# Kernel optimization log

Hardware: AMD Instinct MI355X
Metric: run time of the kernel (lower is better)

The kernel has to match this reference:

```python
import jax, jax.numpy as jnp
import numpy as np

NUM_ANCHORS_LIST = [6400, 1600, 400]  # 640x640 input, strides 8/16/32
STRIDES = [8, 16, 32]
GRID_SIZES = [80, 40, 20]
TOPK = 9
EPS = 1e-9


def _make_anchor_bboxes():
    boxes = []
    for stride, size in zip(STRIDES, GRID_SIZES):
        c = (np.arange(size, dtype=np.float32) + 0.5) * stride
        cx, cy = np.meshgrid(c, c)
        half = stride / 2.0
        b = np.stack([cx - half, cy - half, cx + half, cy + half], axis=-1)
        boxes.append(b.reshape(-1, 4))
    return jnp.asarray(np.concatenate(boxes, axis=0))  # [8400,4]


def _random_boxes(key, shape_prefix, img=640.0):
    k1, k2 = jax.random.split(key)
    cxy = jax.random.uniform(k1, shape_prefix + (2,), minval=0.0, maxval=img)
    wh = jax.random.uniform(k2, shape_prefix + (2,), minval=8.0, maxval=160.0)
    x1y1 = jnp.clip(cxy - wh / 2, 0.0, img)
    x2y2 = jnp.clip(cxy + wh / 2, 0.0, img)
    return jnp.concatenate([x1y1, x2y2], axis=-1).astype(jnp.float32)


def setup_inputs() -> dict:
    key = jax.random.key(0)
    kg, kp, kl, km = jax.random.split(key, 4)
    B, N, M, C = 16, 8400, 128, 80
    return {
        "anchor_bboxes": _make_anchor_bboxes(),               # [N,4]
        "gt_labels": jax.random.randint(kl, (B, M, 1), 0, C).astype(jnp.int64),
        "gt_bboxes": _random_boxes(kg, (B, M)),               # [B,M,4]
        "mask_gt": jax.random.randint(km, (B, M, 1), 0, 2).astype(jnp.int32),
        "pred_bboxes": _random_boxes(kp, (B, N)),             # [B,N,4]
        "num_classes": C,
    }


def _batch_bbox_iou(box1, box2):
    # box1 [B,N,4], box2 [B,M,4] -> [B,N,M]
    area1 = (box1[..., 2] - box1[..., 0]) * (box1[..., 3] - box1[..., 1])
    area2 = (box2[..., 2] - box2[..., 0]) * (box2[..., 3] - box2[..., 1])
    ix1 = jnp.maximum(box1[:, :, None, 0], box2[:, None, :, 0])
    iy1 = jnp.maximum(box1[:, :, None, 1], box2[:, None, :, 1])
    ix2 = jnp.minimum(box1[:, :, None, 2], box2[:, None, :, 2])
    iy2 = jnp.minimum(box1[:, :, None, 3], box2[:, None, :, 3])
    inter = jnp.maximum(ix2 - ix1, 0.0) * jnp.maximum(iy2 - iy1, 0.0)
    union = area1[:, :, None] + area2[:, None, :] - inter
    return inter / (union + EPS)


def reference(anchor_bboxes, gt_labels, gt_bboxes, mask_gt, pred_bboxes, num_classes):
    B, M = gt_bboxes.shape[0], gt_bboxes.shape[1]
    N = anchor_bboxes.shape[0]
    labels = gt_labels[..., 0].astype(jnp.int32)           # [B,M]

    ac = (anchor_bboxes[:, :2] + anchor_bboxes[:, 2:]) / 2  # [N,2]
    gc = (gt_bboxes[..., :2] + gt_bboxes[..., 2:]) / 2      # [B,M,2]
    # cdist via expanded quadratic form (avoids [B,N,M,2] intermediate)
    a2 = jnp.sum(ac * ac, axis=-1)                          # [N]
    g2 = jnp.sum(gc * gc, axis=-1)                          # [B,M]
    d2 = a2[None, :, None] + g2[:, None, :] - 2.0 * jnp.einsum('nc,bmc->bnm', ac, gc)
    distances = jnp.sqrt(jnp.maximum(d2, 0.0))              # [B,N,M]

    # per-level topk closest anchors per GT -> candidate mask [B,N,M]
    bidx = jnp.arange(B)[:, None, None]
    midx = jnp.arange(M)[None, :, None]
    level_masks = []
    start = 0
    for ln in NUM_ANCHORS_LIST:
        ld = distances[:, start:start + ln, :]               # [B,ln,M]
        k = min(TOPK, ln)
        _, idx = jax.lax.top_k(-jnp.swapaxes(ld, 1, 2), k)   # [B,M,k] anchor idx
        lm = jnp.zeros((B, ln, M), dtype=bool).at[bidx, idx, midx].set(True)
        level_masks.append(lm)
        start += ln
    candidate_mask = jnp.concatenate(level_masks, axis=1)    # [B,N,M]

    ious = _batch_bbox_iou(jnp.broadcast_to(anchor_bboxes[None], (B, N, 4)), gt_bboxes)
    cm_f = candidate_mask.astype(ious.dtype)
    cand_ious = ious * cm_f
    count = jnp.maximum(cm_f.sum(axis=1), 1.0)               # [B,M]
    mean = cand_ious.sum(axis=1) / count
    sq_mean = jnp.sum(cand_ious * cand_ious, axis=1) / count # mask is 0/1
    std = jnp.sqrt(jnp.maximum(sq_mean - mean * mean, 0.0))
    thr = mean + std                                         # [B,M]

    is_pos = candidate_mask & (ious >= thr[:, None, :])
    center_in_gt = ((ac[None, :, None, 0] >= gt_bboxes[:, None, :, 0])
                    & (ac[None, :, None, 0] <= gt_bboxes[:, None, :, 2])
                    & (ac[None, :, None, 1] >= gt_bboxes[:, None, :, 1])
                    & (ac[None, :, None, 1] <= gt_bboxes[:, None, :, 3]))
    is_pos = is_pos & center_in_gt & (mask_gt[..., 0] > 0)[:, None, :]

    fg_mask = jnp.any(is_pos, axis=-1)                       # [B,N]
    pos_ious = jnp.where(is_pos, ious, 0.0)
    max_gt_idx = jnp.argmax(pos_ious, axis=-1)               # [B,N]

    fg_f = fg_mask.astype(ious.dtype)
    assigned_labels = jnp.take_along_axis(labels, max_gt_idx, axis=1) * fg_mask.astype(jnp.int32)
    assigned_bboxes = jnp.take_along_axis(gt_bboxes, max_gt_idx[..., None], axis=1) * fg_f[..., None]
    assigned_ious = jnp.take_along_axis(ious, max_gt_idx[..., None], axis=2)[..., 0] * fg_f

    pred_ious = _batch_bbox_iou(pred_bboxes, gt_bboxes)
    pred_assigned = jnp.take_along_axis(pred_ious, max_gt_idx[..., None], axis=2)[..., 0] * fg_f
    assigned_ious = assigned_ious * pred_assigned

    assigned_scores = jax.nn.one_hot(assigned_labels, num_classes, dtype=ious.dtype) \
        * (assigned_ious * fg_f)[..., None]                  # [B,N,C]
    return assigned_labels, assigned_bboxes, assigned_scores, fg_mask
```

## Files before the change

kernel.cpp:

```cpp
#include <hip/hip_runtime.h>
#include <stdint.h>

#define B_ 16
#define N_ 8400
#define M_ 128
#define SC4_  2688000
#define ZB_   512
#define ZPER_ 5250

__device__ __forceinline__ float iou_box(float ax1, float ay1, float ax2, float ay2,
                                         float bx1, float by1, float bx2, float by2) {
    float area1 = __fmul_rn(__fsub_rn(ax2, ax1), __fsub_rn(ay2, ay1));
    float area2 = __fmul_rn(__fsub_rn(bx2, bx1), __fsub_rn(by2, by1));
    float ix1 = fmaxf(ax1, bx1), iy1 = fmaxf(ay1, by1);
    float ix2 = fminf(ax2, bx2), iy2 = fminf(ay2, by2);
    float iw = fmaxf(__fsub_rn(ix2, ix1), 0.0f);
    float ih = fmaxf(__fsub_rn(iy2, iy1), 0.0f);
    float inter = __fmul_rn(iw, ih);
    float uni = __fsub_rn(__fadd_rn(area1, area2), inter);
    return __fdiv_rn(inter, __fadd_rn(uni, 1e-9f));
}

__global__ __launch_bounds__(256) void assign_zero_kernel(
    const float* __restrict__ gt_bboxes,
    const int* __restrict__ mask_gt,
    unsigned long long* __restrict__ ws,
    float* __restrict__ out) {
    if (blockIdx.x >= 2048) {
        float4* sp = (float4*)(out + (size_t)B_ * N_ * 5) +
                     (size_t)(blockIdx.x - 2048) * ZPER_;
        const float4 z4 = make_float4(0.f, 0.f, 0.f, 0.f);
        for (int k = threadIdx.x; k < ZPER_; k += 256) sp[k] = z4;
        return;
    }

    const int g = blockIdx.x;
    if (mask_gt[g] == 0) return;
    const int t = threadIdx.x;
    if (t >= 192) return;
    const int b = g >> 7;
    const int m = g & (M_ - 1);
    const int w = t >> 6;
    const int lane = t & 63;

    __shared__ int   s_idx[27];
    __shared__ float s_iou[27];
    __shared__ int   s_cin[27];
    __shared__ float s_thr;

    const float4 gb = ((const float4*)gt_bboxes)[g];
    const float gx1 = gb.x, gy1 = gb.y, gx2 = gb.z, gy2 = gb.w;
    const float gcx = __fmul_rn(__fadd_rn(gx1, gx2), 0.5f);
    const float gcy = __fmul_rn(__fadd_rn(gy1, gy2), 0.5f);
    const float g2 = __fadd_rn(__fmul_rn(gcx, gcx), __fmul_rn(gcy, gcy));

    const int   size  = (w == 0) ? 80 : ((w == 1) ? 40 : 20);
    const int   start = (w == 0) ? 0 : ((w == 1) ? 6400 : 8000);
    const float st    = (w == 0) ? 8.0f : ((w == 1) ? 16.0f : 32.0f);
    const float inv   = (w == 0) ? 0.125f : ((w == 1) ? 0.0625f : 0.03125f);

    int jl = (int)floorf(gcx * inv - 0.5f) - 2;
    int il = (int)floorf(gcy * inv - 0.5f) - 2;
    jl = min(max(jl, 0), size - 6);
    il = min(max(il, 0), size - 6);

    unsigned long long key = ~0ULL;
    if (lane < 36) {
        const int wy = lane / 6;
        const int wx = lane - wy * 6;
        const int   i   = il + wy;
        const int   j   = jl + wx;
        const float acy = __fmul_rn(__fadd_rn((float)i, 0.5f), st);
        const float acx = __fmul_rn(__fadd_rn((float)j, 0.5f), st);
        const int   n   = start + i * size + j;
        float a2  = __fadd_rn(__fmul_rn(acx, acx), __fmul_rn(acy, acy));
        float dot = __fadd_rn(__fmul_rn(acx, gcx), __fmul_rn(acy, gcy));
        float d2  = __fsub_rn(__fadd_rn(a2, g2), __fmul_rn(2.0f, dot));
        float dist = __fsqrt_rn(fmaxf(d2, 0.0f));
        key = ((unsigned long long)__float_as_uint(dist) << 32) | (unsigned)n;
    }

#pragma unroll
    for (int k = 2; k <= 64; k <<= 1) {
#pragma unroll
        for (int j = k >> 1; j > 0; j >>= 1) {
            unsigned long long other = __shfl_xor(key, j, 64);
            const bool up = ((lane & k) == 0);
            const bool keepMin = (((lane & j) == 0) == up);
            const unsigned long long mn = key < other ? key : other;
            const unsigned long long mx = key < other ? other : key;
            key = keepMin ? mn : mx;
        }
    }
    if (lane < 9) s_idx[w * 9 + lane] = (int)(key & 0xFFFFFFFFu);
    __syncthreads();

    if (t < 3) {
        int v[9];
#pragma unroll
        for (int k = 0; k < 9; ++k) v[k] = s_idx[t * 9 + k];
#pragma unroll
        for (int rr = 0; rr < 9; ++rr) {
#pragma unroll
            for (int p = (rr & 1); p + 1 < 9; p += 2) {
                int lo = min(v[p], v[p + 1]);
                int hi = max(v[p], v[p + 1]);
                v[p] = lo; v[p + 1] = hi;
            }
        }
#pragma unroll
        for (int k = 0; k < 9; ++k) s_idx[t * 9 + k] = v[k];
    }
    __syncthreads();

    if (t < 27) {
        const int   l      = t / 9;
        const int   size2  = (l == 0) ? 80 : ((l == 1) ? 40 : 20);
        const int   start2 = (l == 0) ? 0 : ((l == 1) ? 6400 : 8000);
        const float st2    = (l == 0) ? 8.0f : ((l == 1) ? 16.0f : 32.0f);
        const float half   = __fmul_rn(st2, 0.5f);
        const int n = s_idx[t];
        const int loc = n - start2;
        const int i = loc / size2;
        const int j = loc - i * size2;
        float acx = __fmul_rn(__fadd_rn((float)j, 0.5f), st2);
        float acy = __fmul_rn(__fadd_rn((float)i, 0.5f), st2);
        float ax1 = __fsub_rn(acx, half), ay1 = __fsub_rn(acy, half);
        float ax2 = __fadd_rn(acx, half), ay2 = __fadd_rn(acy, half);
        float iou = iou_box(ax1, ay1, ax2, ay2, gx1, gy1, gx2, gy2);
        s_iou[t] = iou;
        s_cin[t] = (acx >= gx1 && acx <= gx2 && acy >= gy1 && acy <= gy2) ? 1 : 0;
    }
    __syncthreads();

    if (t == 0) {
        float tot = 0.0f, tot2 = 0.0f;
#pragma unroll
        for (int kk = 0; kk < 27; ++kk) {
            const float iou = s_iou[kk];
            tot  = __fadd_rn(tot, iou);
            tot2 = __fadd_rn(tot2, __fmul_rn(iou, iou));
        }
        float mean = __fdiv_rn(tot, 27.0f);
        float sqm  = __fdiv_rn(tot2, 27.0f);
        float var  = __fsub_rn(sqm, __fmul_rn(mean, mean));
        float stdv = __fsqrt_rn(fmaxf(var, 0.0f));
        s_thr = __fadd_rn(mean, stdv);
    }
    __syncthreads();

    if (t < 27) {
        const float iou = s_iou[t];
        if (s_cin[t] && iou >= s_thr) {
            unsigned long long packed =
                ((unsigned long long)(0xC0000000u | __float_as_uint(iou)) << 32) |
                (unsigned long long)(0xFFFFFFFFu - (unsigned)m);
            atomicMax(&ws[(size_t)b * N_ + s_idx[t]], packed);
        }
    }
}

__global__ __launch_bounds__(256) void finalize_kernel(
    const int* __restrict__ gt_labels,
    const float* __restrict__ gt_bboxes,
    const float* __restrict__ pred_bboxes,
    const int* __restrict__ num_classes_p,
    const unsigned long long* __restrict__ ws,
    float* __restrict__ out) {
    const int idx = blockIdx.x * 256 + threadIdx.x;
    const int b = idx / N_;
    const int C = num_classes_p[0];

    const unsigned long long w = ws[idx];
    const bool fg = (w >> 62) == 3ULL;
    float labelf = 0.0f;
    float4 bb = make_float4(0.f, 0.f, 0.f, 0.f);
    float v = 0.0f, fgf = 0.0f;
    int label = 0;
    if (fg) {
        fgf = 1.0f;
        const unsigned mm = 0xFFFFFFFFu - (unsigned)(w & 0xFFFFFFFFu);
        const float a_iou = __uint_as_float((unsigned)((w >> 32) & 0x3FFFFFFFu));
        label = gt_labels[b * M_ + (int)mm];
        labelf = (float)label;
        const float* gg = gt_bboxes + ((size_t)b * M_ + mm) * 4;
        bb.x = gg[0]; bb.y = gg[1]; bb.z = gg[2]; bb.w = gg[3];
        const float* p = pred_bboxes + (size_t)idx * 4;
        float piou = iou_box(p[0], p[1], p[2], p[3], bb.x, bb.y, bb.z, bb.w);
        v = __fmul_rn(a_iou, piou);
    }

    out[idx] = labelf;
    ((float4*)(out + (size_t)B_ * N_))[idx] = bb;
    if (fg) out[(size_t)B_ * N_ * 5 + (size_t)idx * C + label] = v;
    out[(size_t)B_ * N_ * (5 + C) + idx] = fgf;
}

extern "C" void kernel_launch(void* const* d_in, const int* in_sizes, int n_in,
                              void* d_out, int out_size, void* d_ws, size_t ws_size,
                              hipStream_t stream) {
    const int*   gt_labels  = (const int*)d_in[1];
    const float* gt_bboxes  = (const float*)d_in[2];
    const int*   mask_gt    = (const int*)d_in[3];
    const float* pred       = (const float*)d_in[4];
    const int*   ncls       = (const int*)d_in[5];
    unsigned long long* ws  = (unsigned long long*)d_ws;
    float* out              = (float*)d_out;

    assign_zero_kernel<<<2048 + ZB_, 256, 0, stream>>>(gt_bboxes, mask_gt, ws, out);
    finalize_kernel<<<(B_ * N_) / 256, 256, 0, stream>>>(
        gt_labels, gt_bboxes, pred, ncls, ws, out);
}
```

Baseline: 82.91 us.

## Fuse assignment, output zeroing, and finalize into one cooperative kernel

Merges the per-GT assignment kernel and the per-anchor finalize kernel into a single cooperative launch of 2048 blocks. A grid-wide sync separates the two phases. Zeroing of the whole output now happens in each block's fourth wave, alongside the assignment work. The finalize phase now writes only foreground anchors because everything was pre-zeroed. This removes one kernel launch and the dense writes of background entries, at the cost of a grid barrier and a requirement that all 2048 blocks be co-resident.

```diff
diff --git a/kernel.cpp b/kernel.cpp
--- a/kernel.cpp
+++ b/kernel.cpp
@@ -1,12 +1,14 @@
 #include <hip/hip_runtime.h>
+#include <hip/hip_cooperative_groups.h>
 #include <stdint.h>
+
+namespace cg = cooperative_groups;
 
 #define B_ 16
 #define N_ 8400
 #define M_ 128
-#define SC4_  2688000
-#define ZB_   512
-#define ZPER_ 5250
+#define OUT4_ 2889600
+#define ZPER_ 1411
 
 __device__ __forceinline__ float iou_box(float ax1, float ay1, float ax2, float ay2,
                                          float bx1, float by1, float bx2, float by2) {
@@ -21,81 +23,90 @@
     return __fdiv_rn(inter, __fadd_rn(uni, 1e-9f));
 }
 
-__global__ __launch_bounds__(256) void assign_zero_kernel(
+__global__ __launch_bounds__(256, 8) void fused_coop_kernel(
+    const int* __restrict__ gt_labels,
     const float* __restrict__ gt_bboxes,
     const int* __restrict__ mask_gt,
+    const float* __restrict__ pred_bboxes,
+    const int* __restrict__ num_classes_p,
     unsigned long long* __restrict__ ws,
     float* __restrict__ out) {
-    if (blockIdx.x >= 2048) {
-        float4* sp = (float4*)(out + (size_t)B_ * N_ * 5) +
-                     (size_t)(blockIdx.x - 2048) * ZPER_;
-        const float4 z4 = make_float4(0.f, 0.f, 0.f, 0.f);
-        for (int k = threadIdx.x; k < ZPER_; k += 256) sp[k] = z4;
-        return;
-    }
-
+    cg::grid_group grid = cg::this_grid();
     const int g = blockIdx.x;
-    if (mask_gt[g] == 0) return;
     const int t = threadIdx.x;
-    if (t >= 192) return;
+    const bool activeGT = (mask_gt[g] != 0);
     const int b = g >> 7;
     const int m = g & (M_ - 1);
-    const int w = t >> 6;
-    const int lane = t & 63;
 
     __shared__ int   s_idx[27];
     __shared__ float s_iou[27];
     __shared__ int   s_cin[27];
     __shared__ float s_thr;
 
-    const float4 gb = ((const float4*)gt_bboxes)[g];
-    const float gx1 = gb.x, gy1 = gb.y, gx2 = gb.z, gy2 = gb.w;
-    const float gcx = __fmul_rn(__fadd_rn(gx1, gx2), 0.5f);
-    const float gcy = __fmul_rn(__fadd_rn(gy1, gy2), 0.5f);
-    const float g2 = __fadd_rn(__fmul_rn(gcx, gcx), __fmul_rn(gcy, gcy));
-
-    const int   size  = (w == 0) ? 80 : ((w == 1) ? 40 : 20);
-    const int   start = (w == 0) ? 0 : ((w == 1) ? 6400 : 8000);
-    const float st    = (w == 0) ? 8.0f : ((w == 1) ? 16.0f : 32.0f);
-    const float inv   = (w == 0) ? 0.125f : ((w == 1) ? 0.0625f : 0.03125f);
-
-    int jl = (int)floorf(gcx * inv - 0.5f) - 2;
-    int il = (int)floorf(gcy * inv - 0.5f) - 2;
-    jl = min(max(jl, 0), size - 6);
-    il = min(max(il, 0), size - 6);
-
-    unsigned long long key = ~0ULL;
-    if (lane < 36) {
-        const int wy = lane / 6;
-        const int wx = lane - wy * 6;
-        const int   i   = il + wy;
-        const int   j   = jl + wx;
-        const float acy = __fmul_rn(__fadd_rn((float)i, 0.5f), st);
-        const float acx = __fmul_rn(__fadd_rn((float)j, 0.5f), st);
-        const int   n   = start + i * size + j;
-        float a2  = __fadd_rn(__fmul_rn(acx, acx), __fmul_rn(acy, acy));
-        float dot = __fadd_rn(__fmul_rn(acx, gcx), __fmul_rn(acy, gcy));
-        float d2  = __fsub_rn(__fadd_rn(a2, g2), __fmul_rn(2.0f, dot));
-        float dist = __fsqrt_rn(fmaxf(d2, 0.0f));
-        key = ((unsigned long long)__float_as_uint(dist) << 32) | (unsigned)n;
-    }
-
-#pragma unroll
-    for (int k = 2; k <= 64; k <<= 1) {
-#pragma unroll
-        for (int j = k >> 1; j > 0; j >>= 1) {
-            unsigned long long other = __shfl_xor(key, j, 64);
-            const bool up = ((lane & k) == 0);
-            const bool keepMin = (((lane & j) == 0) == up);
-            const unsigned long long mn = key < other ? key : other;
-            const unsigned long long mx = key < other ? other : key;
-            key = keepMin ? mn : mx;
-        }
-    }
-    if (lane < 9) s_idx[w * 9 + lane] = (int)(key & 0xFFFFFFFFu);
-    __syncthreads();
-
-    if (t < 3) {
+    float gx1 = 0.f, gy1 = 0.f, gx2 = 0.f, gy2 = 0.f;
+    if (activeGT) {
+        const float4 gb = ((const float4*)gt_bboxes)[g];
+        gx1 = gb.x; gy1 = gb.y; gx2 = gb.z; gy2 = gb.w;
+    }
+
+    if (t >= 192) {
+        float4* o4 = (float4*)out;
+        const float4 z4 = make_float4(0.f, 0.f, 0.f, 0.f);
+        const int base = g * ZPER_;
+        for (int k = t - 192; k < ZPER_; k += 64) {
+            const int i = base + k;
+            if (i < OUT4_) o4[i] = z4;
+        }
+    } else if (activeGT) {
+        const int w = t >> 6;
+        const int lane = t & 63;
+        const float gcx = __fmul_rn(__fadd_rn(gx1, gx2), 0.5f);
+        const float gcy = __fmul_rn(__fadd_rn(gy1, gy2), 0.5f);
+        const float g2 = __fadd_rn(__fmul_rn(gcx, gcx), __fmul_rn(gcy, gcy));
+
+        const int   size  = (w == 0) ? 80 : ((w == 1) ? 40 : 20);
+        const int   start = (w == 0) ? 0 : ((w == 1) ? 6400 : 8000);
+        const float st    = (w == 0) ? 8.0f : ((w == 1) ? 16.0f : 32.0f);
+        const float inv   = (w == 0) ? 0.125f : ((w == 1) ? 0.0625f : 0.03125f);
+
+        int jl = (int)floorf(gcx * inv - 0.5f) - 2;
+        int il = (int)floorf(gcy * inv - 0.5f) - 2;
+        jl = min(max(jl, 0), size - 6);
+        il = min(max(il, 0), size - 6);
+
+        unsigned long long key = ~0ULL;
+        if (lane < 36) {
+            const int wy = lane / 6;
+            const int wx = lane - wy * 6;
+            const int   i   = il + wy;
+            const int   j   = jl + wx;
+            const float acy = __fmul_rn(__fadd_rn((float)i, 0.5f), st);
+            const float acx = __fmul_rn(__fadd_rn((float)j, 0.5f), st);
+            const int   n   = start + i * size + j;
+            float a2  = __fadd_rn(__fmul_rn(acx, acx), __fmul_rn(acy, acy));
+            float dot = __fadd_rn(__fmul_rn(acx, gcx), __fmul_rn(acy, gcy));
+            float d2  = __fsub_rn(__fadd_rn(a2, g2), __fmul_rn(2.0f, dot));
+            float dist = __fsqrt_rn(fmaxf(d2, 0.0f));
+            key = ((unsigned long long)__float_as_uint(dist) << 32) | (unsigned)n;
+        }
+
+#pragma unroll
+        for (int k = 2; k <= 64; k <<= 1) {
+#pragma unroll
+            for (int j = k >> 1; j > 0; j >>= 1) {
+                unsigned long long other = __shfl_xor(key, j, 64);
+                const bool up = ((lane & k) == 0);
+                const bool keepMin = (((lane & j) == 0) == up);
+                const unsigned long long mn = key < other ? key : other;
+                const unsigned long long mx = key < other ? other : key;
+                key = keepMin ? mn : mx;
+            }
+        }
+        if (lane < 9) s_idx[w * 9 + lane] = (int)(key & 0xFFFFFFFFu);
+    }
+    __syncthreads();
+
+    if (activeGT && t < 3) {
         int v[9];
 #pragma unroll
         for (int k = 0; k < 9; ++k) v[k] = s_idx[t * 9 + k];
@@ -113,7 +124,7 @@
     }
     __syncthreads();
 
-    if (t < 27) {
+    if (activeGT && t < 27) {
         const int   l      = t / 9;
         const int   size2  = (l == 0) ? 80 : ((l == 1) ? 40 : 20);
         const int   start2 = (l == 0) ? 0 : ((l == 1) ? 6400 : 8000);
@@ -133,7 +144,7 @@
     }
     __syncthreads();
 
-    if (t == 0) {
+    if (activeGT && t == 0) {
         float tot = 0.0f, tot2 = 0.0f;
 #pragma unroll
         for (int kk = 0; kk < 27; ++kk) {
@@ -149,7 +160,7 @@
     }
     __syncthreads();
 
-    if (t < 27) {
+    if (activeGT && t < 27) {
         const float iou = s_iou[t];
         if (s_cin[t] && iou >= s_thr) {
             unsigned long long packed =
@@ -158,42 +169,32 @@
             atomicMax(&ws[(size_t)b * N_ + s_idx[t]], packed);
         }
     }
-}
-
-__global__ __launch_bounds__(256) void finalize_kernel(
-    const int* __restrict__ gt_labels,
-    const float* __restrict__ gt_bboxes,
-    const float* __restrict__ pred_bboxes,
-    const int* __restrict__ num_classes_p,
-    const unsigned long long* __restrict__ ws,
-    float* __restrict__ out) {
-    const int idx = blockIdx.x * 256 + threadIdx.x;
-    const int b = idx / N_;
+
+    grid.sync();
+
     const int C = num_classes_p[0];
-
-    const unsigned long long w = ws[idx];
-    const bool fg = (w >> 62) == 3ULL;
-    float labelf = 0.0f;
-    float4 bb = make_float4(0.f, 0.f, 0.f, 0.f);
-    float v = 0.0f, fgf = 0.0f;
-    int label = 0;
-    if (fg) {
-        fgf = 1.0f;
-        const unsigned mm = 0xFFFFFFFFu - (unsigned)(w & 0xFFFFFFFFu);
-        const float a_iou = __uint_as_float((unsigned)((w >> 32) & 0x3FFFFFFFu));
-        label = gt_labels[b * M_ + (int)mm];
-        labelf = (float)label;
-        const float* gg = gt_bboxes + ((size_t)b * M_ + mm) * 4;
-        bb.x = gg[0]; bb.y = gg[1]; bb.z = gg[2]; bb.w = gg[3];
-        const float* p = pred_bboxes + (size_t)idx * 4;
-        float piou = iou_box(p[0], p[1], p[2], p[3], bb.x, bb.y, bb.z, bb.w);
-        v = __fmul_rn(a_iou, piou);
-    }
-
-    out[idx] = labelf;
-    ((float4*)(out + (size_t)B_ * N_))[idx] = bb;
-    if (fg) out[(size_t)B_ * N_ * 5 + (size_t)idx * C + label] = v;
-    out[(size_t)B_ * N_ * (5 + C) + idx] = fgf;
+    if (t < 66) {
+        const int idx = g * 66 + t;
+        if (idx < B_ * N_) {
+            const unsigned long long w = atomicAdd(&ws[idx], 0ULL);
+            if ((w >> 62) == 3ULL) {
+                const int bb_ = idx / N_;
+                const unsigned mm = 0xFFFFFFFFu - (unsigned)(w & 0xFFFFFFFFu);
+                const float a_iou = __uint_as_float((unsigned)((w >> 32) & 0x3FFFFFFFu));
+                const int label = gt_labels[bb_ * M_ + (int)mm];
+                const float* gg = gt_bboxes + ((size_t)bb_ * M_ + mm) * 4;
+                float4 bbv;
+                bbv.x = gg[0]; bbv.y = gg[1]; bbv.z = gg[2]; bbv.w = gg[3];
+                const float* p = pred_bboxes + (size_t)idx * 4;
+                float piou = iou_box(p[0], p[1], p[2], p[3], bbv.x, bbv.y, bbv.z, bbv.w);
+                const float v = __fmul_rn(a_iou, piou);
+                out[idx] = (float)label;
+                ((float4*)(out + (size_t)B_ * N_))[idx] = bbv;
+                out[(size_t)B_ * N_ * 5 + (size_t)idx * C + label] = v;
+                out[(size_t)B_ * N_ * (5 + C) + idx] = 1.0f;
+            }
+        }
+    }
 }
 
 extern "C" void kernel_launch(void* const* d_in, const int* in_sizes, int n_in,
@@ -207,7 +208,8 @@
     unsigned long long* ws  = (unsigned long long*)d_ws;
     float* out              = (float*)d_out;
 
-    assign_zero_kernel<<<2048 + ZB_, 256, 0, stream>>>(gt_bboxes, mask_gt, ws, out);
-    finalize_kernel<<<(B_ * N_) / 256, 256, 0, stream>>>(
-        gt_labels, gt_bboxes, pred, ncls, ws, out);
+    void* args[] = {(void*)&gt_labels, (void*)&gt_bboxes, (void*)&mask_gt,
+                    (void*)&pred, (void*)&ncls, (void*)&ws, (void*)&out};
+    hipLaunchCooperativeKernel((const void*)fused_coop_kernel,
+                               dim3(B_ * M_), dim3(256), args, 0, stream);
 }
```

After: 285.1 us. +243.8%, slower.

## Spread output zeroing across all blocks and write only foreground in finalize

Applied to the files above, without the earlier changes.

The whole output buffer (labels, boxes, scores, fg mask) is now zeroed by every block of the assign kernel. Each block zeroes its own slice after its assignment work, so the 2048 assign blocks now also store data instead of leaving 512 dedicated blocks to do it. The finalize kernel returns early for background anchors and writes label, box, score and fg only for foreground ones, which removes most of its stores. The cost is a larger zeroing pass, since it now also covers the label, box and fg regions, and 64 extra threads in each assign block that wait at the barriers.

```diff
diff --git a/kernel.cpp b/kernel.cpp
--- a/kernel.cpp
+++ b/kernel.cpp
@@ -4,9 +4,9 @@
 #define B_ 16
 #define N_ 8400
 #define M_ 128
-#define SC4_  2688000
-#define ZB_   512
-#define ZPER_ 5250
+#define OUT4_ 2889600
+#define NB_   2560
+#define ZPER_ 1129
 
 __device__ __forceinline__ float iou_box(float ax1, float ay1, float ax2, float ay2,
                                          float bx1, float by1, float bx2, float by2) {
@@ -26,136 +26,142 @@
     const int* __restrict__ mask_gt,
     unsigned long long* __restrict__ ws,
     float* __restrict__ out) {
-    if (blockIdx.x >= 2048) {
-        float4* sp = (float4*)(out + (size_t)B_ * N_ * 5) +
-                     (size_t)(blockIdx.x - 2048) * ZPER_;
+    const int g = blockIdx.x;
+    const int t = threadIdx.x;
+    const bool doAssign = (g < 2048) && (mask_gt[g < 2048 ? g : 0] != 0);
+
+    if (doAssign) {
+        const int b = g >> 7;
+        const int m = g & (M_ - 1);
+
+        __shared__ int   s_idx[27];
+        __shared__ float s_iou[27];
+        __shared__ int   s_cin[27];
+        __shared__ float s_thr;
+
+        const float4 gb = ((const float4*)gt_bboxes)[g];
+        const float gx1 = gb.x, gy1 = gb.y, gx2 = gb.z, gy2 = gb.w;
+        const float gcx = __fmul_rn(__fadd_rn(gx1, gx2), 0.5f);
+        const float gcy = __fmul_rn(__fadd_rn(gy1, gy2), 0.5f);
+        const float g2 = __fadd_rn(__fmul_rn(gcx, gcx), __fmul_rn(gcy, gcy));
+
+        if (t < 192) {
+            const int w = t >> 6;
+            const int lane = t & 63;
+            const int   size  = (w == 0) ? 80 : ((w == 1) ? 40 : 20);
+            const int   start = (w == 0) ? 0 : ((w == 1) ? 6400 : 8000);
+            const float st    = (w == 0) ? 8.0f : ((w == 1) ? 16.0f : 32.0f);
+            const float inv   = (w == 0) ? 0.125f : ((w == 1) ? 0.0625f : 0.03125f);
+
+            int jl = (int)floorf(gcx * inv - 0.5f) - 2;
+            int il = (int)floorf(gcy * inv - 0.5f) - 2;
+            jl = min(max(jl, 0), size - 6);
+            il = min(max(il, 0), size - 6);
+
+            unsigned long long key = ~0ULL;
+            if (lane < 36) {
+                const int wy = lane / 6;
+                const int wx = lane - wy * 6;
+                const int   i   = il + wy;
+                const int   j   = jl + wx;
+                const float acy = __fmul_rn(__fadd_rn((float)i, 0.5f), st);
+                const float acx = __fmul_rn(__fadd_rn((float)j, 0.5f), st);
+                const int   n   = start + i * size + j;
+                float a2  = __fadd_rn(__fmul_rn(acx, acx), __fmul_rn(acy, acy));
+                float dot = __fadd_rn(__fmul_rn(acx, gcx), __fmul_rn(acy, gcy));
+                float d2  = __fsub_rn(__fadd_rn(a2, g2), __fmul_rn(2.0f, dot));
+                float dist = __fsqrt_rn(fmaxf(d2, 0.0f));
+                key = ((unsigned long long)__float_as_uint(dist) << 32) | (unsigned)n;
+            }
+#pragma unroll
+            for (int k = 2; k <= 64; k <<= 1) {
+#pragma unroll
+                for (int j = k >> 1; j > 0; j >>= 1) {
+                    unsigned long long other = __shfl_xor(key, j, 64);
+                    const bool up = ((lane & k) == 0);
+                    const bool keepMin = (((lane & j) == 0) == up);
+                    const unsigned long long mn = key < other ? key : other;
+                    const unsigned long long mx = key < other ? other : key;
+                    key = keepMin ? mn : mx;
+                }
+            }
+            if (lane < 9) s_idx[w * 9 + lane] = (int)(key & 0xFFFFFFFFu);
+        }
+        __syncthreads();
+
+        if (t < 3) {
+            int v[9];
+#pragma unroll
+            for (int k = 0; k < 9; ++k) v[k] = s_idx[t * 9 + k];
+#pragma unroll
+            for (int rr = 0; rr < 9; ++rr) {
+#pragma unroll
+                for (int p = (rr & 1); p + 1 < 9; p += 2) {
+                    int lo = min(v[p], v[p + 1]);
+                    int hi = max(v[p], v[p + 1]);
+                    v[p] = lo; v[p + 1] = hi;
+                }
+            }
+#pragma unroll
+            for (int k = 0; k < 9; ++k) s_idx[t * 9 + k] = v[k];
+        }
+        __syncthreads();
+
+        if (t < 27) {
+            const int   l      = t / 9;
+            const int   size2  = (l == 0) ? 80 : ((l == 1) ? 40 : 20);
+            const int   start2 = (l == 0) ? 0 : ((l == 1) ? 6400 : 8000);
+            const float st2    = (l == 0) ? 8.0f : ((l == 1) ? 16.0f : 32.0f);
+            const float half   = __fmul_rn(st2, 0.5f);
+            const int n = s_idx[t];
+            const int loc = n - start2;
+            const int i = loc / size2;
+            const int j = loc - i * size2;
+            float acx = __fmul_rn(__fadd_rn((float)j, 0.5f), st2);
+            float acy = __fmul_rn(__fadd_rn((float)i, 0.5f), st2);
+            float ax1 = __fsub_rn(acx, half), ay1 = __fsub_rn(acy, half);
+            float ax2 = __fadd_rn(acx, half), ay2 = __fadd_rn(acy, half);
+            float iou = iou_box(ax1, ay1, ax2, ay2, gx1, gy1, gx2, gy2);
+            s_iou[t] = iou;
+            s_cin[t] = (acx >= gx1 && acx <= gx2 && acy >= gy1 && acy <= gy2) ? 1 : 0;
+        }
+        __syncthreads();
+
+        if (t == 0) {
+            float tot = 0.0f, tot2 = 0.0f;
+#pragma unroll
+            for (int kk = 0; kk < 27; ++kk) {
+                const float iou = s_iou[kk];
+                tot  = __fadd_rn(tot, iou);
+                tot2 = __fadd_rn(tot2, __fmul_rn(iou, iou));
+            }
+            float mean = __fdiv_rn(tot, 27.0f);
+            float sqm  = __fdiv_rn(tot2, 27.0f);
+            float var  = __fsub_rn(sqm, __fmul_rn(mean, mean));
+            float stdv = __fsqrt_rn(fmaxf(var, 0.0f));
+            s_thr = __fadd_rn(mean, stdv);
+        }
+        __syncthreads();
+
+        if (t < 27) {
+            const float iou = s_iou[t];
+            if (s_cin[t] && iou >= s_thr) {
+                unsigned long long packed =
+                    ((unsigned long long)(0xC0000000u | __float_as_uint(iou)) << 32) |
+                    (unsigned long long)(0xFFFFFFFFu - (unsigned)m);
+                atomicMax(&ws[(size_t)b * N_ + s_idx[t]], packed);
+            }
+        }
+    }
+
+    {
+        float4* o4 = (float4*)out;
         const float4 z4 = make_float4(0.f, 0.f, 0.f, 0.f);
-        for (int k = threadIdx.x; k < ZPER_; k += 256) sp[k] = z4;
-        return;
-    }
-
-    const int g = blockIdx.x;
-    if (mask_gt[g] == 0) return;
-    const int t = threadIdx.x;
-    if (t >= 192) return;
-    const int b = g >> 7;
-    const int m = g & (M_ - 1);
-    const int w = t >> 6;
-    const int lane = t & 63;
-
-    __shared__ int   s_idx[27];
-    __shared__ float s_iou[27];
-    __shared__ int   s_cin[27];
-    __shared__ float s_thr;
-
-    const float4 gb = ((const float4*)gt_bboxes)[g];
-    const float gx1 = gb.x, gy1 = gb.y, gx2 = gb.z, gy2 = gb.w;
-    const float gcx = __fmul_rn(__fadd_rn(gx1, gx2), 0.5f);
-    const float gcy = __fmul_rn(__fadd_rn(gy1, gy2), 0.5f);
-    const float g2 = __fadd_rn(__fmul_rn(gcx, gcx), __fmul_rn(gcy, gcy));
-
-    const int   size  = (w == 0) ? 80 : ((w == 1) ? 40 : 20);
-    const int   start = (w == 0) ? 0 : ((w == 1) ? 6400 : 8000);
-    const float st    = (w == 0) ? 8.0f : ((w == 1) ? 16.0f : 32.0f);
-    const float inv   = (w == 0) ? 0.125f : ((w == 1) ? 0.0625f : 0.03125f);
-
-    int jl = (int)floorf(gcx * inv - 0.5f) - 2;
-    int il = (int)floorf(gcy * inv - 0.5f) - 2;
-    jl = min(max(jl, 0), size - 6);
-    il = min(max(il, 0), size - 6);
-
-    unsigned long long key = ~0ULL;
-    if (lane < 36) {
-        const int wy = lane / 6;
-        const int wx = lane - wy * 6;
-        const int   i   = il + wy;
-        const int   j   = jl + wx;
-        const float acy = __fmul_rn(__fadd_rn((float)i, 0.5f), st);
-        const float acx = __fmul_rn(__fadd_rn((float)j, 0.5f), st);
-        const int   n   = start + i * size + j;
-        float a2  = __fadd_rn(__fmul_rn(acx, acx), __fmul_rn(acy, acy));
-        float dot = __fadd_rn(__fmul_rn(acx, gcx), __fmul_rn(acy, gcy));
-        float d2  = __fsub_rn(__fadd_rn(a2, g2), __fmul_rn(2.0f, dot));
-        float dist = __fsqrt_rn(fmaxf(d2, 0.0f));
-        key = ((unsigned long long)__float_as_uint(dist) << 32) | (unsigned)n;
-    }
-
-#pragma unroll
-    for (int k = 2; k <= 64; k <<= 1) {
-#pragma unroll
-        for (int j = k >> 1; j > 0; j >>= 1) {
-            unsigned long long other = __shfl_xor(key, j, 64);
-            const bool up = ((lane & k) == 0);
-            const bool keepMin = (((lane & j) == 0) == up);
-            const unsigned long long mn = key < other ? key : other;
-            const unsigned long long mx = key < other ? other : key;
-            key = keepMin ? mn : mx;
-        }
-    }
-    if (lane < 9) s_idx[w * 9 + lane] = (int)(key & 0xFFFFFFFFu);
-    __syncthreads();
-
-    if (t < 3) {
-        int v[9];
-#pragma unroll
-        for (int k = 0; k < 9; ++k) v[k] = s_idx[t * 9 + k];
-#pragma unroll
-        for (int rr = 0; rr < 9; ++rr) {
-#pragma unroll
-            for (int p = (rr & 1); p + 1 < 9; p += 2) {
-                int lo = min(v[p], v[p + 1]);
-                int hi = max(v[p], v[p + 1]);
-                v[p] = lo; v[p + 1] = hi;
-            }
-        }
-#pragma unroll
-        for (int k = 0; k < 9; ++k) s_idx[t * 9 + k] = v[k];
-    }
-    __syncthreads();
-
-    if (t < 27) {
-        const int   l      = t / 9;
-        const int   size2  = (l == 0) ? 80 : ((l == 1) ? 40 : 20);
-        const int   start2 = (l == 0) ? 0 : ((l == 1) ? 6400 : 8000);
-        const float st2    = (l == 0) ? 8.0f : ((l == 1) ? 16.0f : 32.0f);
-        const float half   = __fmul_rn(st2, 0.5f);
-        const int n = s_idx[t];
-        const int loc = n - start2;
-        const int i = loc / size2;
-        const int j = loc - i * size2;
-        float acx = __fmul_rn(__fadd_rn((float)j, 0.5f), st2);
-        float acy = __fmul_rn(__fadd_rn((float)i, 0.5f), st2);
-        float ax1 = __fsub_rn(acx, half), ay1 = __fsub_rn(acy, half);
-        float ax2 = __fadd_rn(acx, half), ay2 = __fadd_rn(acy, half);
-        float iou = iou_box(ax1, ay1, ax2, ay2, gx1, gy1, gx2, gy2);
-        s_iou[t] = iou;
-        s_cin[t] = (acx >= gx1 && acx <= gx2 && acy >= gy1 && acy <= gy2) ? 1 : 0;
-    }
-    __syncthreads();
-
-    if (t == 0) {
-        float tot = 0.0f, tot2 = 0.0f;
-#pragma unroll
-        for (int kk = 0; kk < 27; ++kk) {
-            const float iou = s_iou[kk];
-            tot  = __fadd_rn(tot, iou);
-            tot2 = __fadd_rn(tot2, __fmul_rn(iou, iou));
-        }
-        float mean = __fdiv_rn(tot, 27.0f);
-        float sqm  = __fdiv_rn(tot2, 27.0f);
-        float var  = __fsub_rn(sqm, __fmul_rn(mean, mean));
-        float stdv = __fsqrt_rn(fmaxf(var, 0.0f));
-        s_thr = __fadd_rn(mean, stdv);
-    }
-    __syncthreads();
-
-    if (t < 27) {
-        const float iou = s_iou[t];
-        if (s_cin[t] && iou >= s_thr) {
-            unsigned long long packed =
-                ((unsigned long long)(0xC0000000u | __float_as_uint(iou)) << 32) |
-                (unsigned long long)(0xFFFFFFFFu - (unsigned)m);
-            atomicMax(&ws[(size_t)b * N_ + s_idx[t]], packed);
+        const int base = g * ZPER_;
+#pragma unroll
+        for (int k = 0; k < 5; ++k) {
+            const int i = base + t + k * 256;
+            if (i < base + ZPER_ && i < OUT4_) o4[i] = z4;
         }
     }
 }
@@ -168,32 +174,25 @@
     const unsigned long long* __restrict__ ws,
     float* __restrict__ out) {
     const int idx = blockIdx.x * 256 + threadIdx.x;
+    const unsigned long long w = ws[idx];
+    if ((w >> 62) != 3ULL) return;
     const int b = idx / N_;
     const int C = num_classes_p[0];
 
-    const unsigned long long w = ws[idx];
-    const bool fg = (w >> 62) == 3ULL;
-    float labelf = 0.0f;
-    float4 bb = make_float4(0.f, 0.f, 0.f, 0.f);
-    float v = 0.0f, fgf = 0.0f;
-    int label = 0;
-    if (fg) {
-        fgf = 1.0f;
-        const unsigned mm = 0xFFFFFFFFu - (unsigned)(w & 0xFFFFFFFFu);
-        const float a_iou = __uint_as_float((unsigned)((w >> 32) & 0x3FFFFFFFu));
-        label = gt_labels[b * M_ + (int)mm];
-        labelf = (float)label;
-        const float* gg = gt_bboxes + ((size_t)b * M_ + mm) * 4;
-        bb.x = gg[0]; bb.y = gg[1]; bb.z = gg[2]; bb.w = gg[3];
-        const float* p = pred_bboxes + (size_t)idx * 4;
-        float piou = iou_box(p[0], p[1], p[2], p[3], bb.x, bb.y, bb.z, bb.w);
-        v = __fmul_rn(a_iou, piou);
-    }
-
-    out[idx] = labelf;
-    ((float4*)(out + (size_t)B_ * N_))[idx] = bb;
-    if (fg) out[(size_t)B_ * N_ * 5 + (size_t)idx * C + label] = v;
-    out[(size_t)B_ * N_ * (5 + C) + idx] = fgf;
+    const unsigned mm = 0xFFFFFFFFu - (unsigned)(w & 0xFFFFFFFFu);
+    const float a_iou = __uint_as_float((unsigned)((w >> 32) & 0x3FFFFFFFu));
+    const int label = gt_labels[b * M_ + (int)mm];
+    const float* gg = gt_bboxes + ((size_t)b * M_ + mm) * 4;
+    float4 bbv;
+    bbv.x = gg[0]; bbv.y = gg[1]; bbv.z = gg[2]; bbv.w = gg[3];
+    const float* p = pred_bboxes + (size_t)idx * 4;
+    float piou = iou_box(p[0], p[1], p[2], p[3], bbv.x, bbv.y, bbv.z, bbv.w);
+    const float v = __fmul_rn(a_iou, piou);
+
+    out[idx] = (float)label;
+    ((float4*)(out + (size_t)B_ * N_))[idx] = bbv;
+    out[(size_t)B_ * N_ * 5 + (size_t)idx * C + label] = v;
+    out[(size_t)B_ * N_ * (5 + C) + idx] = 1.0f;
 }
 
 extern "C" void kernel_launch(void* const* d_in, const int* in_sizes, int n_in,
@@ -207,7 +206,7 @@
     unsigned long long* ws  = (unsigned long long*)d_ws;
     float* out              = (float*)d_out;
 
-    assign_zero_kernel<<<2048 + ZB_, 256, 0, stream>>>(gt_bboxes, mask_gt, ws, out);
+    assign_zero_kernel<<<NB_, 256, 0, stream>>>(gt_bboxes, mask_gt, ws, out);
     finalize_kernel<<<(B_ * N_) / 256, 256, 0, stream>>>(
         gt_labels, gt_bboxes, pred, ncls, ws, out);
 }
```

New measurement: 83.17 us. About the same (+0.3%).
